# Kernel optimization log

Hardware: AMD Instinct MI355X
Metric: run time of the kernel (lower is better)

The kernel has to match this reference:

```python
import jax, jax.numpy as jnp
import numpy as np
import math

NUM_POINTS = 9
DILATION = 1
STRIDE = 1
BN_EPS = 1e-5


def _initial_offsets(p):
    g = int(math.ceil(math.sqrt(p)))
    c = (g - 1) / 2.0
    offs = [[i - c, j - c] for i in range(g) for j in range(g)][:p]
    return jnp.asarray(offs, dtype=jnp.float32)  # [P,2] = (dy, dx)


def _bilinear_sample(x, sy, sx):
    # x: [B,C,H,W]; sy, sx: [B,H,W,P] float pixel coords.
    # Zero padding for out-of-bounds corners (matches grid_sample zeros + align_corners=True).
    B, C, H, W = x.shape
    y0 = jnp.floor(sy); x0 = jnp.floor(sx)
    y1 = y0 + 1.0;      x1 = x0 + 1.0
    wy1 = sy - y0; wy0 = 1.0 - wy1
    wx1 = sx - x0; wx0 = 1.0 - wx1
    xf = x.reshape(B, C, H * W)

    def gather(yi, xi):
        valid = ((yi >= 0) & (yi < H) & (xi >= 0) & (xi < W)).astype(x.dtype)
        yc = jnp.clip(yi, 0, H - 1).astype(jnp.int32)
        xc = jnp.clip(xi, 0, W - 1).astype(jnp.int32)
        idx = (yc * W + xc).reshape(B, 1, -1)              # [B,1,H*W*P]
        v = jnp.take_along_axis(xf, idx, axis=2)           # [B,C,H*W*P]
        return v * valid.reshape(B, 1, -1)

    out = (gather(y0, x0) * (wy0 * wx0).reshape(B, 1, -1)
         + gather(y0, x1) * (wy0 * wx1).reshape(B, 1, -1)
         + gather(y1, x0) * (wy1 * wx0).reshape(B, 1, -1)
         + gather(y1, x1) * (wy1 * wx1).reshape(B, 1, -1))
    return out  # [B,C,H*W*P]


def _akconv(x, dw_w, dw_b, bn_gamma, bn_beta, bn_mean, bn_var, pw_w, pw_b, weight, bias):
    B, C, H, W = x.shape
    P = NUM_POINTS
    # offset branch: depthwise 3x3 conv -> BN (eval mode) -> SiLU -> 1x1 conv
    h = jax.lax.conv_general_dilated(x, dw_w, (1, 1), ((1, 1), (1, 1)),
                                     dimension_numbers=('NCHW', 'OIHW', 'NCHW'),
                                     feature_group_count=C)
    h = h + dw_b[None, :, None, None]
    inv = jax.lax.rsqrt(bn_var + BN_EPS)
    h = (h - bn_mean[None, :, None, None]) * (bn_gamma * inv)[None, :, None, None] + bn_beta[None, :, None, None]
    h = h * jax.nn.sigmoid(h)  # SiLU
    off = jax.lax.conv_general_dilated(h, pw_w, (1, 1), ((0, 0), (0, 0)),
                                       dimension_numbers=('NCHW', 'OIHW', 'NCHW'))
    off = off + pw_b[None, :, None, None]                       # [B,2P,H,W]
    off = off.reshape(B, P, 2, H, W).transpose(0, 3, 4, 1, 2)   # [B,H,W,P,2]
    off = (off + _initial_offsets(P)[None, None, None]) * DILATION
    gy = jnp.arange(H, dtype=x.dtype)[None, :, None, None]
    gx = jnp.arange(W, dtype=x.dtype)[None, None, :, None]
    sy = gy + off[..., 0]                                       # [B,H,W,P]
    sx = gx + off[..., 1]
    # (normalize-to-[-1,1] then grid_sample(align_corners=True) cancels exactly -> sample at pixel coords)
    sampled = _bilinear_sample(x, sy, sx).reshape(B, C, H * W, P)
    out = jnp.einsum('bcnp,ocp->bno', sampled, weight) + bias   # [B,HW,O]
    out = out.reshape(B, H, W, -1).transpose(0, 3, 1, 2)        # [B,O,H,W]
    if STRIDE > 1:
        out = out[:, :, ::STRIDE, ::STRIDE]
    return out


def setup_inputs() -> dict:
    key = jax.random.key(0)
    ks = jax.random.split(key, 8)
    B, C, O, H, W, P = 8, 64, 64, 128, 128, NUM_POINTS
    x = jax.random.normal(ks[0], (B, C, H, W), dtype=jnp.float32)
    dw_w = jax.random.normal(ks[1], (C, 1, 3, 3), dtype=jnp.float32) * 0.1
    dw_b = jax.random.normal(ks[2], (C,), dtype=jnp.float32) * 0.05
    bn_gamma = jnp.ones((C,), dtype=jnp.float32)
    bn_beta = jnp.zeros((C,), dtype=jnp.float32)
    bn_mean = jnp.zeros((C,), dtype=jnp.float32)
    bn_var = jnp.ones((C,), dtype=jnp.float32)
    pw_w = jax.random.normal(ks[3], (2 * P, C, 1, 1), dtype=jnp.float32) * 0.01
    pw_b = jnp.zeros((2 * P,), dtype=jnp.float32)
    weight = jax.random.normal(ks[4], (O, C, P), dtype=jnp.float32) * 0.05
    bias = jax.random.normal(ks[5], (O,), dtype=jnp.float32) * 0.05
    return {"x": x, "dw_w": dw_w, "dw_b": dw_b, "bn_gamma": bn_gamma, "bn_beta": bn_beta,
            "bn_mean": bn_mean, "bn_var": bn_var, "pw_w": pw_w, "pw_b": pw_b,
            "weight": weight, "bias": bias}


def reference(x, dw_w, dw_b, bn_gamma, bn_beta, bn_mean, bn_var, pw_w, pw_b, weight, bias):
    return _akconv(x, dw_w, dw_b, bn_gamma, bn_beta, bn_mean, bn_var, pw_w, pw_b, weight, bias)
```

## Files before the change

kernel.cpp:

```cpp
#include <hip/hip_runtime.h>
#include <math.h>

#define BB 8
#define CC 64
#define OO 64
#define HH 128
#define WW 128
#define PP 9
#define HWIMG 16384
#define NTOT  131072

typedef __attribute__((ext_vector_type(8))) _Float16 h8;
typedef __attribute__((ext_vector_type(2))) _Float16 h2;
typedef __attribute__((ext_vector_type(4))) float f32x4;
typedef __attribute__((ext_vector_type(4))) unsigned int u32x4;

__global__ void k_prep(const float* __restrict__ w,
                       const float* __restrict__ dw_w,
                       const float* __restrict__ dw_b,
                       const float* __restrict__ gamma,
                       const float* __restrict__ beta,
                       const float* __restrict__ mean,
                       const float* __restrict__ var,
                       const float* __restrict__ pw_w,
                       const float* __restrict__ pw_b,
                       _Float16* __restrict__ wtf2,
                       float* __restrict__ dwt,
                       float* __restrict__ bnA,
                       float* __restrict__ bnB,
                       _Float16* __restrict__ pwa,
                       float* __restrict__ pwb) {
  int bid = blockIdx.x, t = threadIdx.x;
  if (bid < 144) {
    int i = bid * 256 + t;
    int e  = i & 7;
    int ln = (i >> 3) & 63;
    int kc = (i >> 9) & 1;
    int mt = (i >> 10) & 3;
    int p  = i >> 12;
    int o = mt * 16 + (ln & 15);
    int c = kc * 32 + (ln >> 4) * 8 + e;
    wtf2[i] = (_Float16)w[(o * 64 + c) * 9 + p];
  } else {
    if (t < 64) {
      float A = gamma[t] * rsqrtf(var[t] + 1e-5f);
      bnA[t] = A;
      bnB[t] = (dw_b[t] - mean[t]) * A + beta[t];
    }
    if (t < 32) pwb[t] = (t < 18) ? pw_b[t] : 0.f;
    for (int i = t; i < 576; i += 256) {
      int tap = i % 9, c = i / 9;
      dwt[tap * 64 + c] = dw_w[c * 9 + tap];
    }
    for (int i = t; i < 2048; i += 256) {
      int e  = i & 7;
      int ln = (i >> 3) & 63;
      int kc = (i >> 9) & 1;
      int mt = (i >> 10) & 1;
      int ko = mt * 16 + (ln & 15);
      int c  = kc * 32 + ((ln >> 4) & 3) * 8 + e;
      pwa[i] = (ko < 18) ? (_Float16)pw_w[ko * 64 + c] : (_Float16)0.f;
    }
  }
}

__global__ void __launch_bounds__(256, 4)
k_tr(const float* __restrict__ x, _Float16* __restrict__ xt) {
  __shared__ _Float16 lt[64][66];
  int bid = blockIdx.x;
  int vbid = (bid & 7) * 256 + (bid >> 3);
  int tid = threadIdx.x;
  int wid = tid >> 6, ln = tid & 63;
  int b = vbid >> 8;
  int pix0 = (vbid & 255) * 64;
  const float* xbb = x + (size_t)b * CC * HWIMG;

  #pragma unroll
  for (int i = 0; i < 8; ++i) {
    int c0 = (wid * 8 + i) * 2;
    float v0 = xbb[(size_t)c0 * HWIMG + pix0 + ln];
    float v1 = xbb[(size_t)(c0 + 1) * HWIMG + pix0 + ln];
    h2 hv;
    hv[0] = (_Float16)v0;
    hv[1] = (_Float16)v1;
    *(h2*)&lt[ln][c0] = hv;
  }
  __syncthreads();

  int pq = tid >> 2, q = tid & 3;
  h8 o0, o1;
  #pragma unroll
  for (int j = 0; j < 4; ++j) {
    h2 v = *(h2*)&lt[pq][q * 16 + 2 * j];
    o0[2 * j] = v[0];
    o0[2 * j + 1] = v[1];
  }
  #pragma unroll
  for (int j = 0; j < 4; ++j) {
    h2 v = *(h2*)&lt[pq][q * 16 + 8 + 2 * j];
    o1[2 * j] = v[0];
    o1[2 * j + 1] = v[1];
  }
  _Float16* op = xt + ((size_t)((b << 14) + pix0 + pq)) * 64 + q * 16;
  *(h8*)op = o0;
  *(h8*)(op + 8) = o1;
}

template<bool BORDER>
__device__ __forceinline__ void tile_body(
    const _Float16* __restrict__ xb,
    const float* __restrict__ dwt,
    const float* __restrict__ bnA,
    const float* __restrict__ bnB,
    const _Float16* __restrict__ pwa,
    const float* __restrict__ pwb,
    const _Float16* __restrict__ wtf2,
    const float* __restrict__ bias,
    float* __restrict__ out,
    char* smem, int b, int ty0, int tx0, int tid) {
  char* off_lds = smem + 240 * 128;
  int wid = tid >> 6, ln = tid & 63;
  int lm = ln & 15, lk = ln >> 4;

  for (int ch = tid; ch < 1920; ch += 256) {
    int rec = ch >> 3, j = ch & 7;
    int ry = rec / 20, rx = rec - ry * 20;
    int yy = min(max(ty0 - 2 + ry, 0), HH - 1);
    int xx = min(max(tx0 - 2 + rx, 0), WW - 1);
    h8 v = *((const h8*)(xb + ((size_t)((yy << 7) + xx)) * 64) + (j ^ (rec & 7)));
    *(h8*)(smem + rec * 128 + j * 16) = v;
  }
  __syncthreads();

  int qy0 = wid * 2;
  int y0r = ty0 + qy0;

  float s[2][16];
  #pragma unroll
  for (int nt = 0; nt < 2; ++nt)
    #pragma unroll
    for (int e = 0; e < 16; ++e) s[nt][e] = 0.f;

  #pragma unroll
  for (int tap = 0; tap < 9; ++tap) {
    int dy = tap / 3 - 1, dx = tap % 3 - 1;
    int xc2 = tx0 + lm + dx;
    bool cok = (xc2 >= 0) & (xc2 < WW);
    const float* dwp = dwt + tap * 64;
    f32x4 d0a = *(const f32x4*)(dwp + lk * 8);
    f32x4 d0b = *(const f32x4*)(dwp + lk * 8 + 4);
    f32x4 d1a = *(const f32x4*)(dwp + 32 + lk * 8);
    f32x4 d1b = *(const f32x4*)(dwp + 32 + lk * 8 + 4);
    #pragma unroll
    for (int nt = 0; nt < 2; ++nt) {
      int rec = (qy0 + nt + dy + 2) * 20 + (lm + dx + 2);
      h8 v0 = *(const h8*)(smem + rec * 128 + (((lk    ) ^ (rec & 7)) << 4));
      h8 v1 = *(const h8*)(smem + rec * 128 + (((lk + 4) ^ (rec & 7)) << 4));
      if (BORDER) {
        int ry = y0r + nt + dy;
        bool ok = cok & (ry >= 0) & (ry < HH);
        if (!ok) { v0 = (h8)(_Float16)0.f; v1 = (h8)(_Float16)0.f; }
      }
      #pragma unroll
      for (int e = 0; e < 4; ++e) {
        s[nt][e]      += d0a[e] * (float)v0[e];
        s[nt][4 + e]  += d0b[e] * (float)v0[4 + e];
        s[nt][8 + e]  += d1a[e] * (float)v1[e];
        s[nt][12 + e] += d1b[e] * (float)v1[4 + e];
      }
    }
  }

  h8 bo[2][2];
  {
    f32x4 ba0 = *(const f32x4*)(bnA + lk * 8);
    f32x4 ba1 = *(const f32x4*)(bnA + lk * 8 + 4);
    f32x4 ba2 = *(const f32x4*)(bnA + 32 + lk * 8);
    f32x4 ba3 = *(const f32x4*)(bnA + 32 + lk * 8 + 4);
    f32x4 bb0 = *(const f32x4*)(bnB + lk * 8);
    f32x4 bb1 = *(const f32x4*)(bnB + lk * 8 + 4);
    f32x4 bb2 = *(const f32x4*)(bnB + 32 + lk * 8);
    f32x4 bb3 = *(const f32x4*)(bnB + 32 + lk * 8 + 4);
    #pragma unroll
    for (int nt = 0; nt < 2; ++nt) {
      #pragma unroll
      for (int e = 0; e < 4; ++e) {
        float v;
        v = s[nt][e]      * ba0[e] + bb0[e];
        s[nt][e]      = v * __builtin_amdgcn_rcpf(1.f + __expf(-v));
        v = s[nt][4 + e]  * ba1[e] + bb1[e];
        s[nt][4 + e]  = v * __builtin_amdgcn_rcpf(1.f + __expf(-v));
        v = s[nt][8 + e]  * ba2[e] + bb2[e];
        s[nt][8 + e]  = v * __builtin_amdgcn_rcpf(1.f + __expf(-v));
        v = s[nt][12 + e] * ba3[e] + bb3[e];
        s[nt][12 + e] = v * __builtin_amdgcn_rcpf(1.f + __expf(-v));
      }
      #pragma unroll
      for (int e = 0; e < 8; ++e) {
        bo[nt][0][e] = (_Float16)s[nt][e];
        bo[nt][1][e] = (_Float16)s[nt][8 + e];
      }
    }
  }

  f32x4 aco[2][2];
  {
    f32x4 c0 = *(const f32x4*)(pwb + lk * 4);
    f32x4 c1 = *(const f32x4*)(pwb + 16 + lk * 4);
    aco[0][0] = c0; aco[0][1] = c0;
    aco[1][0] = c1; aco[1][1] = c1;
  }
  #pragma unroll
  for (int kc = 0; kc < 2; ++kc) {
    #pragma unroll
    for (int mt = 0; mt < 2; ++mt) {
      h8 A = *(const h8*)(pwa + (mt * 2 + kc) * 512 + ln * 8);
      #pragma unroll
      for (int nt = 0; nt < 2; ++nt)
        aco[mt][nt] = __builtin_amdgcn_mfma_f32_16x16x32_f16(A, bo[nt][kc], aco[mt][nt], 0, 0, 0);
    }
  }

  #pragma unroll
  for (int nt = 0; nt < 2; ++nt) {
    int px = (qy0 + nt) * 16 + lm;
    unsigned* op = (unsigned*)(off_lds + px * 48);
    h2 h01, h23;
    h01[0] = (_Float16)aco[0][nt][0];
    h01[1] = (_Float16)aco[0][nt][1];
    h23[0] = (_Float16)aco[0][nt][2];
    h23[1] = (_Float16)aco[0][nt][3];
    op[2 * lk]     = __builtin_bit_cast(unsigned, h01);
    op[2 * lk + 1] = __builtin_bit_cast(unsigned, h23);
    if (lk == 0) {
      h2 h8p;
      h8p[0] = (_Float16)aco[1][nt][0];
      h8p[1] = (_Float16)aco[1][nt][1];
      op[8] = __builtin_bit_cast(unsigned, h8p);
    }
  }
  asm volatile("s_waitcnt lgkmcnt(0)" ::: "memory");

  unsigned ov[2][9];
  #pragma unroll
  for (int nt = 0; nt < 2; ++nt) {
    int px = (qy0 + nt) * 16 + lm;
    const unsigned* rp = (const unsigned*)(off_lds + px * 48);
    u32x4 r0 = *(const u32x4*)rp;
    u32x4 r1 = *(const u32x4*)(rp + 4);
    unsigned r2 = rp[8];
    ov[nt][0] = r0[0]; ov[nt][1] = r0[1]; ov[nt][2] = r0[2]; ov[nt][3] = r0[3];
    ov[nt][4] = r1[0]; ov[nt][5] = r1[1]; ov[nt][6] = r1[2]; ov[nt][7] = r1[3];
    ov[nt][8] = r2;
  }

  f32x4 acc[4][2];
  #pragma unroll
  for (int mt = 0; mt < 4; ++mt)
    #pragma unroll
    for (int nt = 0; nt < 2; ++nt) acc[mt][nt] = (f32x4){0.f, 0.f, 0.f, 0.f};

  const _Float16* wl = wtf2 + ln * 8;

  #pragma unroll
  for (int p = 0; p < PP; ++p) {
    h8 bfr[2][2];
    #pragma unroll
    for (int nt = 0; nt < 2; ++nt) {
      h2 hh = __builtin_bit_cast(h2, ov[nt][p]);
      float sy = (float)hh[0] + (float)(y0r + nt + p / 3 - 1);
      float sx = (float)hh[1] + (float)(tx0 + lm + p % 3 - 1);

      float y0f = floorf(sy), x0f = floorf(sx);
      float wy1 = sy - y0f, wy0 = 1.f - wy1;
      float wx1 = sx - x0f, wx0 = 1.f - wx1;
      int y0 = (int)y0f, x0i = (int)x0f;

      float w00, w01, w10, w11;
      int r00, r01, r10, r11;
      if (BORDER) {
        bool vy0 = (y0 >= 0) & (y0 < HH);
        bool vy1 = (y0 + 1 >= 0) & (y0 + 1 < HH);
        bool vx0 = (x0i >= 0) & (x0i < WW);
        bool vx1 = (x0i + 1 >= 0) & (x0i + 1 < WW);
        w00 = (vy0 && vx0) ? wy0 * wx0 : 0.f;
        w01 = (vy0 && vx1) ? wy0 * wx1 : 0.f;
        w10 = (vy1 && vx0) ? wy1 * wx0 : 0.f;
        w11 = (vy1 && vx1) ? wy1 * wx1 : 0.f;
        int iy0 = min(max(y0 - ty0 + 2, 0), 11);
        int iy1 = min(max(y0 + 1 - ty0 + 2, 0), 11);
        int ix0 = min(max(x0i - tx0 + 2, 0), 19);
        int ix1 = min(max(x0i + 1 - tx0 + 2, 0), 19);
        r00 = iy0 * 20 + ix0; r01 = iy0 * 20 + ix1;
        r10 = iy1 * 20 + ix0; r11 = iy1 * 20 + ix1;
      } else {
        w00 = wy0 * wx0; w01 = wy0 * wx1;
        w10 = wy1 * wx0; w11 = wy1 * wx1;
        int iy0 = y0 - ty0 + 2;
        int ix0 = x0i - tx0 + 2;
        r00 = iy0 * 20 + ix0; r01 = r00 + 1;
        r10 = r00 + 20;       r11 = r00 + 21;
      }

      h8 v00a = *(const h8*)(smem + r00 * 128 + (((lk    ) ^ (r00 & 7)) << 4));
      h8 v00b = *(const h8*)(smem + r00 * 128 + (((lk + 4) ^ (r00 & 7)) << 4));
      h8 v01a = *(const h8*)(smem + r01 * 128 + (((lk    ) ^ (r01 & 7)) << 4));
      h8 v01b = *(const h8*)(smem + r01 * 128 + (((lk + 4) ^ (r01 & 7)) << 4));
      h8 v10a = *(const h8*)(smem + r10 * 128 + (((lk    ) ^ (r10 & 7)) << 4));
      h8 v10b = *(const h8*)(smem + r10 * 128 + (((lk + 4) ^ (r10 & 7)) << 4));
      h8 v11a = *(const h8*)(smem + r11 * 128 + (((lk    ) ^ (r11 & 7)) << 4));
      h8 v11b = *(const h8*)(smem + r11 * 128 + (((lk + 4) ^ (r11 & 7)) << 4));

      h8 w00v = (h8)(_Float16)w00;
      h8 w01v = (h8)(_Float16)w01;
      h8 w10v = (h8)(_Float16)w10;
      h8 w11v = (h8)(_Float16)w11;
      bfr[nt][0] = v00a * w00v + v01a * w01v + v10a * w10v + v11a * w11v;
      bfr[nt][1] = v00b * w00v + v01b * w01v + v10b * w10v + v11b * w11v;
    }

    #pragma unroll
    for (int mt = 0; mt < 4; ++mt) {
      h8 a0 = *(const h8*)(wl + (p * 8 + mt * 2) * 512);
      h8 a1 = *(const h8*)(wl + (p * 8 + mt * 2 + 1) * 512);
      #pragma unroll
      for (int nt = 0; nt < 2; ++nt) {
        acc[mt][nt] = __builtin_amdgcn_mfma_f32_16x16x32_f16(a0, bfr[nt][0], acc[mt][nt], 0, 0, 0);
        acc[mt][nt] = __builtin_amdgcn_mfma_f32_16x16x32_f16(a1, bfr[nt][1], acc[mt][nt], 0, 0, 0);
      }
    }
  }

  #pragma unroll
  for (int nt = 0; nt < 2; ++nt) {
    int pix = ((y0r + nt) << 7) + tx0 + lm;
    #pragma unroll
    for (int mt = 0; mt < 4; ++mt) {
      #pragma unroll
      for (int r = 0; r < 4; ++r) {
        int m = mt * 16 + lk * 4 + r;
        out[((size_t)b * OO + m) * HWIMG + pix] = acc[mt][nt][r] + bias[m];
      }
    }
  }
}

__global__ void __launch_bounds__(256, 4)
k_main(const _Float16* __restrict__ xt,
       const float* __restrict__ dwt,
       const float* __restrict__ bnA,
       const float* __restrict__ bnB,
       const _Float16* __restrict__ pwa,
       const float* __restrict__ pwb,
       const _Float16* __restrict__ wtf2,
       const float* __restrict__ bias,
       float* __restrict__ out) {
  __shared__ __attribute__((aligned(16))) char smem[240 * 128 + 6144];
  int bid = blockIdx.x;
  int b = bid & 7, t = bid >> 3;
  int ty0 = (t >> 3) * 8, tx0 = (t & 7) * 16;
  int tid = threadIdx.x;
  const _Float16* xb = xt + (((size_t)b) << 14) * 64;

  bool border = (ty0 == 0) || (ty0 == 120) || (tx0 == 0) || (tx0 == 112);
  if (border)
    tile_body<true >(xb, dwt, bnA, bnB, pwa, pwb, wtf2, bias, out, smem, b, ty0, tx0, tid);
  else
    tile_body<false>(xb, dwt, bnA, bnB, pwa, pwb, wtf2, bias, out, smem, b, ty0, tx0, tid);
}

extern "C" void kernel_launch(void* const* d_in, const int* in_sizes, int n_in,
                              void* d_out, int out_size, void* d_ws, size_t ws_size,
                              hipStream_t stream) {
  const float* x        = (const float*)d_in[0];
  const float* dw_w     = (const float*)d_in[1];
  const float* dw_b     = (const float*)d_in[2];
  const float* bn_gamma = (const float*)d_in[3];
  const float* bn_beta  = (const float*)d_in[4];
  const float* bn_mean  = (const float*)d_in[5];
  const float* bn_var   = (const float*)d_in[6];
  const float* pw_w     = (const float*)d_in[7];
  const float* pw_b     = (const float*)d_in[8];
  const float* weight   = (const float*)d_in[9];
  const float* bias     = (const float*)d_in[10];
  float* out = (float*)d_out;

  char* ws = (char*)d_ws;
  _Float16* wtf2 = (_Float16*)ws;
  size_t o1 = (size_t)PP * OO * CC * 2;
  _Float16* xtb = (_Float16*)(ws + o1);
  size_t o2 = o1 + (size_t)NTOT * CC * 2;
  float* dwt = (float*)(ws + o2);
  float* bnA = (float*)(ws + o2 + 2304);
  float* bnB = (float*)(ws + o2 + 2304 + 256);
  _Float16* pwa = (_Float16*)(ws + o2 + 2304 + 512);
  float* pwb = (float*)(ws + o2 + 2304 + 512 + 4096);

  k_prep<<<145, 256, 0, stream>>>(weight, dw_w, dw_b, bn_gamma, bn_beta,
                                  bn_mean, bn_var, pw_w, pw_b,
                                  wtf2, dwt, bnA, bnB, pwa, pwb);
  k_tr<<<NTOT / 64, 256, 0, stream>>>(x, xtb);
  k_main<<<NTOT / 128, 256, 0, stream>>>(xtb, dwt, bnA, bnB, pwa, pwb,
                                         wtf2, bias, out);
}
```

Measured before the change: 54.11 us.

## Pad LDS halo rows instead of XOR swizzle and shuffle offsets via registers

Replaces the XOR-swizzled 128-byte LDS record layout with a padded 144-byte stride, which makes the address arithmetic for the depthwise and bilinear gathers simpler. The offset values produced by the MFMA are now redistributed across lanes with __shfl instead of being written to an LDS scratch area and read back. That removes the scratch region and its wait. LDS per block changes from 36864 to 34560 bytes. The padding may change the bank-conflict pattern of the irregular bilinear reads, and the shuffles add cross-lane operations in place of LDS traffic.

```diff
diff --git a/kernel.cpp b/kernel.cpp
--- a/kernel.cpp
+++ b/kernel.cpp
@@ -9,11 +9,11 @@
 #define PP 9
 #define HWIMG 16384
 #define NTOT  131072
+#define RSTR 144
 
 typedef __attribute__((ext_vector_type(8))) _Float16 h8;
 typedef __attribute__((ext_vector_type(2))) _Float16 h2;
 typedef __attribute__((ext_vector_type(4))) float f32x4;
-typedef __attribute__((ext_vector_type(4))) unsigned int u32x4;
 
 __global__ void k_prep(const float* __restrict__ w,
                        const float* __restrict__ dw_w,
@@ -118,7 +118,6 @@
     const float* __restrict__ bias,
     float* __restrict__ out,
     char* smem, int b, int ty0, int tx0, int tid) {
-  char* off_lds = smem + 240 * 128;
   int wid = tid >> 6, ln = tid & 63;
   int lm = ln & 15, lk = ln >> 4;
 
@@ -127,8 +126,8 @@
     int ry = rec / 20, rx = rec - ry * 20;
     int yy = min(max(ty0 - 2 + ry, 0), HH - 1);
     int xx = min(max(tx0 - 2 + rx, 0), WW - 1);
-    h8 v = *((const h8*)(xb + ((size_t)((yy << 7) + xx)) * 64) + (j ^ (rec & 7)));
-    *(h8*)(smem + rec * 128 + j * 16) = v;
+    h8 v = *((const h8*)(xb + ((size_t)((yy << 7) + xx)) * 64) + j);
+    *(h8*)(smem + rec * RSTR + j * 16) = v;
   }
   __syncthreads();
 
@@ -154,8 +153,8 @@
     #pragma unroll
     for (int nt = 0; nt < 2; ++nt) {
       int rec = (qy0 + nt + dy + 2) * 20 + (lm + dx + 2);
-      h8 v0 = *(const h8*)(smem + rec * 128 + (((lk    ) ^ (rec & 7)) << 4));
-      h8 v1 = *(const h8*)(smem + rec * 128 + (((lk + 4) ^ (rec & 7)) << 4));
+      h8 v0 = *(const h8*)(smem + rec * RSTR + (lk    ) * 16);
+      h8 v1 = *(const h8*)(smem + rec * RSTR + (lk + 4) * 16);
       if (BORDER) {
         int ry = y0r + nt + dy;
         bool ok = cok & (ry >= 0) & (ry < HH);
@@ -221,37 +220,30 @@
     }
   }
 
+  unsigned pk0[2], pk1[2], pk2[2];
   #pragma unroll
   for (int nt = 0; nt < 2; ++nt) {
-    int px = (qy0 + nt) * 16 + lm;
-    unsigned* op = (unsigned*)(off_lds + px * 48);
-    h2 h01, h23;
-    h01[0] = (_Float16)aco[0][nt][0];
-    h01[1] = (_Float16)aco[0][nt][1];
-    h23[0] = (_Float16)aco[0][nt][2];
-    h23[1] = (_Float16)aco[0][nt][3];
-    op[2 * lk]     = __builtin_bit_cast(unsigned, h01);
-    op[2 * lk + 1] = __builtin_bit_cast(unsigned, h23);
-    if (lk == 0) {
-      h2 h8p;
-      h8p[0] = (_Float16)aco[1][nt][0];
-      h8p[1] = (_Float16)aco[1][nt][1];
-      op[8] = __builtin_bit_cast(unsigned, h8p);
-    }
-  }
-  asm volatile("s_waitcnt lgkmcnt(0)" ::: "memory");
+    h2 a, b2, c;
+    a[0]  = (_Float16)aco[0][nt][0]; a[1]  = (_Float16)aco[0][nt][1];
+    b2[0] = (_Float16)aco[0][nt][2]; b2[1] = (_Float16)aco[0][nt][3];
+    c[0]  = (_Float16)aco[1][nt][0]; c[1]  = (_Float16)aco[1][nt][1];
+    pk0[nt] = __builtin_bit_cast(unsigned, a);
+    pk1[nt] = __builtin_bit_cast(unsigned, b2);
+    pk2[nt] = __builtin_bit_cast(unsigned, c);
+  }
 
   unsigned ov[2][9];
   #pragma unroll
   for (int nt = 0; nt < 2; ++nt) {
-    int px = (qy0 + nt) * 16 + lm;
-    const unsigned* rp = (const unsigned*)(off_lds + px * 48);
-    u32x4 r0 = *(const u32x4*)rp;
-    u32x4 r1 = *(const u32x4*)(rp + 4);
-    unsigned r2 = rp[8];
-    ov[nt][0] = r0[0]; ov[nt][1] = r0[1]; ov[nt][2] = r0[2]; ov[nt][3] = r0[3];
-    ov[nt][4] = r1[0]; ov[nt][5] = r1[1]; ov[nt][6] = r1[2]; ov[nt][7] = r1[3];
-    ov[nt][8] = r2;
+    ov[nt][0] = __shfl(pk0[nt], 0 * 16 + lm);
+    ov[nt][1] = __shfl(pk1[nt], 0 * 16 + lm);
+    ov[nt][2] = __shfl(pk0[nt], 1 * 16 + lm);
+    ov[nt][3] = __shfl(pk1[nt], 1 * 16 + lm);
+    ov[nt][4] = __shfl(pk0[nt], 2 * 16 + lm);
+    ov[nt][5] = __shfl(pk1[nt], 2 * 16 + lm);
+    ov[nt][6] = __shfl(pk0[nt], 3 * 16 + lm);
+    ov[nt][7] = __shfl(pk1[nt], 3 * 16 + lm);
+    ov[nt][8] = __shfl(pk2[nt], lm);
   }
 
   f32x4 acc[4][2];
@@ -302,14 +294,14 @@
         r10 = r00 + 20;       r11 = r00 + 21;
       }
 
-      h8 v00a = *(const h8*)(smem + r00 * 128 + (((lk    ) ^ (r00 & 7)) << 4));
-      h8 v00b = *(const h8*)(smem + r00 * 128 + (((lk + 4) ^ (r00 & 7)) << 4));
-      h8 v01a = *(const h8*)(smem + r01 * 128 + (((lk    ) ^ (r01 & 7)) << 4));
-      h8 v01b = *(const h8*)(smem + r01 * 128 + (((lk + 4) ^ (r01 & 7)) << 4));
-      h8 v10a = *(const h8*)(smem + r10 * 128 + (((lk    ) ^ (r10 & 7)) << 4));
-      h8 v10b = *(const h8*)(smem + r10 * 128 + (((lk + 4) ^ (r10 & 7)) << 4));
-      h8 v11a = *(const h8*)(smem + r11 * 128 + (((lk    ) ^ (r11 & 7)) << 4));
-      h8 v11b = *(const h8*)(smem + r11 * 128 + (((lk + 4) ^ (r11 & 7)) << 4));
+      h8 v00a = *(const h8*)(smem + r00 * RSTR + (lk    ) * 16);
+      h8 v00b = *(const h8*)(smem + r00 * RSTR + (lk + 4) * 16);
+      h8 v01a = *(const h8*)(smem + r01 * RSTR + (lk    ) * 16);
+      h8 v01b = *(const h8*)(smem + r01 * RSTR + (lk + 4) * 16);
+      h8 v10a = *(const h8*)(smem + r10 * RSTR + (lk    ) * 16);
+      h8 v10b = *(const h8*)(smem + r10 * RSTR + (lk + 4) * 16);
+      h8 v11a = *(const h8*)(smem + r11 * RSTR + (lk    ) * 16);
+      h8 v11b = *(const h8*)(smem + r11 * RSTR + (lk + 4) * 16);
 
       h8 w00v = (h8)(_Float16)w00;
       h8 w01v = (h8)(_Float16)w01;
@@ -355,7 +347,7 @@
        const _Float16* __restrict__ wtf2,
        const float* __restrict__ bias,
        float* __restrict__ out) {
-  __shared__ __attribute__((aligned(16))) char smem[240 * 128 + 6144];
+  __shared__ __attribute__((aligned(16))) char smem[240 * RSTR];
   int bid = blockIdx.x;
   int b = bid & 7, t = bid >> 3;
   int ty0 = (t >> 3) * 8, tx0 = (t & 7) * 16;
```

New measurement: 51.87 us, median of 2. 4.1% less time.
